# Optimization experiments

Measured on AMD Instinct MI355X. Metric: run time of the kernel, lower is better.

## Reference

```python
import jax, jax.numpy as jnp
import numpy as np

# Dims: B docs, L tokens, D hidden, H heads, NE padded entities (min_height),
# M mentions per entity, P entity pairs per doc, BLK bilinear block, NL labels.
B, L, D, H, NE, M, P = 4, 1024, 768, 12, 42, 4, 512
BLK, NL = 64, 97
OFFSET = 1  # self.offset = 1 (CLS token shift)


def setup_inputs() -> dict:
    key = jax.random.key(0)
    ks = jax.random.split(key, 10)
    sequence_output = jax.random.normal(ks[0], (B, L, D), jnp.float32)
    att = jax.random.uniform(ks[1], (B, H, L, L), jnp.float32)
    attention = att / att.sum(-1, keepdims=True)  # row-stochastic like softmax attn
    mention_pos = jax.random.randint(ks[2], (B, NE, M), 0, 1000, dtype=jnp.int32)
    hts = jax.random.randint(ks[3], (B, P, 2), 0, NE, dtype=jnp.int32)
    W_head = jax.random.normal(ks[4], (2 * D, D), jnp.float32) * 0.02
    b_head = jnp.zeros((D,), jnp.float32)
    W_tail = jax.random.normal(ks[5], (2 * D, D), jnp.float32) * 0.02
    b_tail = jnp.zeros((D,), jnp.float32)
    W_bi = jax.random.normal(ks[6], (D * BLK, NL), jnp.float32) * 0.02
    b_bi = jnp.zeros((NL,), jnp.float32)
    return dict(sequence_output=sequence_output, attention=attention,
                mention_pos=mention_pos, hts=hts,
                W_head=W_head, b_head=b_head, W_tail=W_tail, b_tail=b_tail,
                W_bi=W_bi, b_bi=b_bi)


def reference(sequence_output, attention, mention_pos, hts,
              W_head, b_head, W_tail, b_tail, W_bi, b_bi):
    pos = mention_pos + OFFSET                               # [B,NE,M]
    # --- get_hrt: entity embeds = logsumexp over mention start tokens ---
    e_emb = jax.vmap(lambda s, p: s[p])(sequence_output, pos)    # [B,NE,M,D]
    entity_embs = jax.nn.logsumexp(e_emb, axis=2)                # [B,NE,D]
    # entity attention = mean over mentions of attn rows           [B,NE,H,L]
    e_att = jax.vmap(lambda a, p: a[:, p])(attention, pos)       # [B,H,NE,M,L]
    entity_atts = e_att.mean(3).transpose(0, 2, 1, 3)            # [B,NE,H,L]
    # --- get_channel_map: ht_att = (h_att * t_att).mean(heads), normalized ---
    ht_att = jnp.einsum('bihl,bjhl->bijl', entity_atts, entity_atts) / H  # [B,NE,NE,L]
    ht_att = ht_att / (ht_att.sum(-1, keepdims=True) + 1e-5)
    rs_map = jnp.einsum('bijl,bld->bijd', ht_att, sequence_output)        # [B,NE,NE,D]
    # --- gather head/tail entity embeds and pooled context per pair ---
    h_idx, t_idx = hts[..., 0], hts[..., 1]                      # [B,P]
    hs = jnp.take_along_axis(entity_embs, h_idx[..., None], axis=1)  # [B,P,D]
    ts = jnp.take_along_axis(entity_embs, t_idx[..., None], axis=1)  # [B,P,D]
    rs = jax.vmap(lambda m, h, t: m[h, t])(rs_map, h_idx, t_idx)     # [B,P,D]
    # --- extractors + grouped bilinear classifier ---
    zs = jnp.tanh(jnp.concatenate([hs, rs], -1) @ W_head + b_head)   # [B,P,D]
    zo = jnp.tanh(jnp.concatenate([ts, rs], -1) @ W_tail + b_tail)   # [B,P,D]
    b1 = zs.reshape(B, P, D // BLK, BLK)
    b2 = zo.reshape(B, P, D // BLK, BLK)
    bl = (b1[..., :, None] * b2[..., None, :]).reshape(B, P, D * BLK)
    logits = bl @ W_bi + b_bi                                        # [B,P,NL]
    return logits
```

## Files before the change

kernel.cpp:

```cpp
#include <hip/hip_runtime.h>

constexpr int Bc = 4, Lc = 1024, Dc = 768, Hc = 12, NEc = 42, Mc = 4, Pc = 512, NLc = 97;
constexpr int BE   = Bc * NEc;
constexpr int BEp  = 176;
constexpr int ROWS = Bc * Pc;
constexpr int N2   = 2 * Dc;

typedef __attribute__((ext_vector_type(8))) short short8;
typedef _Float16 half8 __attribute__((ext_vector_type(8)));
typedef __attribute__((ext_vector_type(4))) float f32x4;

__device__ __forceinline__ f32x4 mfma_bf(short8 a, short8 b, f32x4 c) {
    return __builtin_amdgcn_mfma_f32_16x16x32_bf16(a, b, c, 0, 0, 0);
}
__device__ __forceinline__ f32x4 mfma_h(half8 a, half8 b, f32x4 c) {
    return __builtin_amdgcn_mfma_f32_16x16x32_f16(a, b, c, 0, 0, 0);
}
__device__ __forceinline__ unsigned short f2bf(float x) {
    unsigned int u = __float_as_uint(x);
    return (unsigned short)((u + 0x7fffu + ((u >> 16) & 1u)) >> 16);
}
__device__ __forceinline__ float bf2f(unsigned short h) {
    return __uint_as_float(((unsigned int)h) << 16);
}
__device__ __forceinline__ short8 ld8(const unsigned short* p) {
    return *(const short8*)(const void*)p;
}
__device__ __forceinline__ half8 ldh8(const _Float16* p) {
    return *(const half8*)(const void*)p;
}
__device__ __forceinline__ float fast_tanh(float x) {
    float cx = fminf(fmaxf(x, -9.f), 9.f);
    float u = __expf(2.f * cx);
    return 1.f - 2.f / (u + 1.f);
}


constexpr int PB_EMBS  = 0;
constexpr int PB_EATT  = PB_EMBS + BEp;
constexpr int PB_TRSEQ = PB_EATT + BE * Hc;
constexpr int PB_TRW   = PB_TRSEQ + 768;
constexpr int PB_TRWBI = PB_TRW + 576;
constexpr int PB_ZERO  = PB_TRWBI + 768;
constexpr int PB_TOTAL = PB_ZERO + 97;

__global__ __launch_bounds__(256) void k_prep(const float* __restrict__ seq,
                                              const float* __restrict__ att,
                                              const int* __restrict__ mpos,
                                              const float* __restrict__ Wh,
                                              const float* __restrict__ Wt,
                                              const float* __restrict__ wbi,
                                              unsigned short* __restrict__ ep,
                                              unsigned short* __restrict__ eatt,
                                              unsigned short* __restrict__ sp,
                                              unsigned short* __restrict__ wp1,
                                              unsigned short* __restrict__ wp2,
                                              _Float16* __restrict__ wbp,
                                              float* __restrict__ out_zero) {
    __shared__ float smem[64 * 97];
    int blk = blockIdx.x;
    int t = threadIdx.x;

    if (blk < PB_EATT) {
        int be = blk - PB_EMBS, mt = be >> 4, lm = be & 15;
        float vals[3] = {0.f, 0.f, 0.f};
        if (be < BE) {
            int b = be / NEc;
            const int* pp = mpos + be * Mc;
            int p0 = pp[0] + 1, p1 = pp[1] + 1, p2 = pp[2] + 1, p3 = pp[3] + 1;
            const float* s = seq + (size_t)b * Lc * Dc;
            #pragma unroll
            for (int i = 0; i < 3; ++i) {
                int d = t + i * 256;
                float x0 = s[(size_t)p0 * Dc + d], x1 = s[(size_t)p1 * Dc + d];
                float x2 = s[(size_t)p2 * Dc + d], x3 = s[(size_t)p3 * Dc + d];
                float mx = fmaxf(fmaxf(x0, x1), fmaxf(x2, x3));
                vals[i] = mx + logf(expf(x0 - mx) + expf(x1 - mx) + expf(x2 - mx) + expf(x3 - mx));
            }
        }
        #pragma unroll
        for (int i = 0; i < 3; ++i) {
            int d = t + i * 256;
            int idx = ((mt * 24 + (d >> 5)) << 9) + (((d >> 3) & 3) << 7) + (lm << 3) + (d & 7);
            ep[idx] = f2bf(vals[i]);
        }
    } else if (blk < PB_TRSEQ) {
        int idx = blk - PB_EATT;
        int be = idx / Hc, h = idx - be * Hc, b = be / NEc;
        const int* pp = mpos + be * Mc;
        const float* a = att + ((size_t)(b * Hc + h)) * Lc * Lc;
        const float4* r0 = (const float4*)(a + (size_t)(pp[0] + 1) * Lc);
        const float4* r1 = (const float4*)(a + (size_t)(pp[1] + 1) * Lc);
        const float4* r2 = (const float4*)(a + (size_t)(pp[2] + 1) * Lc);
        const float4* r3 = (const float4*)(a + (size_t)(pp[3] + 1) * Lc);
        unsigned short* o = eatt + ((size_t)be * Hc + h) * Lc;
        float4 v0 = r0[t], v1 = r1[t], v2 = r2[t], v3 = r3[t];
        o[t * 4 + 0] = f2bf(0.25f * (v0.x + v1.x + v2.x + v3.x));
        o[t * 4 + 1] = f2bf(0.25f * (v0.y + v1.y + v2.y + v3.y));
        o[t * 4 + 2] = f2bf(0.25f * (v0.z + v1.z + v2.z + v3.z));
        o[t * 4 + 3] = f2bf(0.25f * (v0.w + v1.w + v2.w + v3.w));
    } else if (blk < PB_TRW) {
        int idx = blk - PB_TRSEQ;
        int xb = idx & 15, yb = (idx >> 4) % 12, b = idx / 192;
        int l0 = xb * 64, d0 = yb * 64;
        const float* s = seq + (size_t)b * Lc * Dc;
        #pragma unroll
        for (int i = 0; i < 16; ++i) {
            int ii = t + i * 256, r = ii >> 6, c = ii & 63;
            smem[r * 65 + c] = s[(size_t)(l0 + r) * Dc + d0 + c];
        }
        __syncthreads();
        unsigned short* outb = sp + (size_t)b * 48 * 32 * 512;
        int flat = t * 2, lane = flat >> 3, j = flat & 7;
        #pragma unroll
        for (int nt_i = 0; nt_i < 4; ++nt_i)
            #pragma unroll
            for (int kb_i = 0; kb_i < 2; ++kb_i) {
                int kl = kb_i * 32 + (lane >> 4) * 8 + j;
                int c  = nt_i * 16 + (lane & 15);
                unsigned int v = (unsigned)f2bf(smem[kl * 65 + c]) |
                                 ((unsigned)f2bf(smem[(kl + 1) * 65 + c]) << 16);
                *(unsigned int*)&outb[(((d0 / 16 + nt_i) * 32 + (l0 / 32 + kb_i)) << 9) + flat] = v;
            }
    } else if (blk < PB_TRWBI) {
        int idx = blk - PB_TRW;
        int xb = idx % 24, yb = (idx / 24) % 12, which = idx / 288;
        int k0 = xb * 64, n0 = yb * 64;
        const float* W = which ? Wt : Wh;
        #pragma unroll
        for (int i = 0; i < 16; ++i) {
            int ii = t + i * 256, r = ii >> 6, c = ii & 63;
            smem[r * 65 + c] = W[(size_t)(k0 + r) * Dc + n0 + c];
        }
        __syncthreads();
        unsigned short* dst = (k0 < Dc) ? wp1 : wp2;
        int kb0 = ((k0 < Dc) ? k0 : (k0 - Dc)) / 32;
        int nt0 = which * 48 + n0 / 16;
        int flat = t * 2, lane = flat >> 3, j = flat & 7;
        #pragma unroll
        for (int nt_i = 0; nt_i < 4; ++nt_i)
            #pragma unroll
            for (int kb_i = 0; kb_i < 2; ++kb_i) {
                int kl = kb_i * 32 + (lane >> 4) * 8 + j;
                int c  = nt_i * 16 + (lane & 15);
                unsigned int v = (unsigned)f2bf(smem[kl * 65 + c]) |
                                 ((unsigned)f2bf(smem[(kl + 1) * 65 + c]) << 16);
                *(unsigned int*)&dst[(((nt0 + nt_i) * 24 + kb0 + kb_i) << 9) + flat] = v;
            }
    } else if (blk < PB_ZERO) {
        int idx = blk - PB_TRWBI;
        int x = idx & 63, g = idx >> 6;
        const float* src = wbi + (size_t)(g * 4096 + x * 64) * NLc;
        for (int i = t; i < 64 * NLc; i += 256) smem[i] = src[i];
        __syncthreads();
        int flat = t * 2, lane = flat >> 3, j = flat & 7;
        int lm = lane & 15, qj = (lane >> 4) * 8 + j;
        #pragma unroll
        for (int nt = 0; nt < 7; ++nt)
            #pragma unroll
            for (int half = 0; half < 2; ++half) {
                int y = half * 32 + qj;
                int n = nt * 16 + lm;
                _Float16 v0 = (n < NLc) ? (_Float16)smem[y * NLc + n] : (_Float16)0.f;
                _Float16 v1 = (n < NLc) ? (_Float16)smem[(y + 1) * NLc + n] : (_Float16)0.f;
                size_t base = ((((size_t)(nt * 12 + g) * 64 + x) * 2 + half) << 9);
                _Float16* d = wbp + base + flat;
                d[0] = v0; d[1] = v1;
            }
    } else {
        int idx = blk - PB_ZERO;
        float4* o = (float4*)(out_zero + (size_t)idx * 2048);
        float4 z = {0.f, 0.f, 0.f, 0.f};
        o[t] = z;
        o[t + 256] = z;
    }
}

__global__ __launch_bounds__(256) void k_pairw(const unsigned short* __restrict__ eatt,
                                               const int* __restrict__ hts,
                                               unsigned short* __restrict__ pwp) {
    int bp = blockIdx.x, b = bp / Pc;
    int hi = hts[bp * 2], ti = hts[bp * 2 + 1];
    const unsigned short* ai = eatt + ((size_t)(b * NEc + hi)) * Hc * Lc;
    const unsigned short* aj = eatt + ((size_t)(b * NEc + ti)) * Hc * Lc;
    int l0 = threadIdx.x * 4;
    float acc[4] = {0.f, 0.f, 0.f, 0.f};
    #pragma unroll
    for (int h = 0; h < Hc; ++h) {
        uint2 ua = *(const uint2*)(ai + h * Lc + l0);
        uint2 ub = *(const uint2*)(aj + h * Lc + l0);
        acc[0] += bf2f(ua.x & 0xffff) * bf2f(ub.x & 0xffff);
        acc[1] += bf2f(ua.x >> 16)    * bf2f(ub.x >> 16);
        acc[2] += bf2f(ua.y & 0xffff) * bf2f(ub.y & 0xffff);
        acc[3] += bf2f(ua.y >> 16)    * bf2f(ub.y >> 16);
    }
    float lsum = acc[0] + acc[1] + acc[2] + acc[3];
    #pragma unroll
    for (int off = 32; off > 0; off >>= 1) lsum += __shfl_down(lsum, off, 64);
    __shared__ float red[4];
    __shared__ float sinv;
    int lane = threadIdx.x & 63, wv = threadIdx.x >> 6;
    if (lane == 0) red[wv] = lsum;
    __syncthreads();
    if (threadIdx.x == 0) sinv = 1.f / (red[0] + red[1] + red[2] + red[3] + 1.2e-4f);
    __syncthreads();
    float s = sinv;
    unsigned short w0 = f2bf(acc[0] * s), w1 = f2bf(acc[1] * s);
    unsigned short w2 = f2bf(acc[2] * s), w3 = f2bf(acc[3] * s);
    int mt = bp >> 4, lm = bp & 15, kb = l0 >> 5, quad = (l0 >> 3) & 3, j0 = l0 & 7;
    unsigned short* dst = pwp + ((mt * 32 + kb) << 9) + (quad << 7) + (lm << 3) + j0;
    *(uint2*)dst = make_uint2((unsigned)w0 | ((unsigned)w1 << 16),
                              (unsigned)w2 | ((unsigned)w3 << 16));
}

__global__ __launch_bounds__(256) void k_rsE(const unsigned short* __restrict__ pwp,
                                             const unsigned short* __restrict__ sp,
                                             const unsigned short* __restrict__ ep,
                                             const unsigned short* __restrict__ wp1,
                                             unsigned short* __restrict__ rsp,
                                             unsigned short* __restrict__ E) {
    int tid = threadIdx.x, wave = tid >> 6, lane = tid & 63;
    int quad = lane >> 4, lm = lane & 15;
    int blk = blockIdx.x;
    if (blk < 384) {
        int mb = blk & 7, ntq = (blk >> 3) % 12, b = blk / 96;
        int nt = ntq * 4 + wave;
        int mt0 = b * 32 + mb * 4;
        const unsigned short* bbase = sp + (((size_t)b * 48 + nt) * 32 << 9) + lane * 8;
        const unsigned short* abase = pwp + ((size_t)mt0 * 32 << 9) + lane * 8;
        f32x4 acc[4] = {};
        for (int kb = 0; kb < 32; ++kb) {
            short8 bf = ld8(bbase + kb * 512);
            #pragma unroll
            for (int mf = 0; mf < 4; ++mf)
                acc[mf] = mfma_bf(ld8(abase + (mf * 32 + kb) * 512), bf, acc[mf]);
        }
        int n = nt * 16 + lm, kbo = n >> 5, lq = ((n >> 3) & 3) << 4, jo = n & 7;
        #pragma unroll
        for (int mf = 0; mf < 4; ++mf) {
            unsigned short* db = rsp + (((mt0 + mf) * 24 + kbo) << 9) + jo;
            #pragma unroll
            for (int r = 0; r < 4; ++r)
                db[(lq + quad * 4 + r) << 3] = f2bf(acc[mf][r]);
        }
    } else {
        int idx = blk - 384;
        int mt = idx % 11, ntq = idx / 11;
        int nt = ntq * 4 + wave;
        const unsigned short* ab = ep + (mt * 24 << 9) + lane * 8;
        const unsigned short* bb = wp1 + (nt * 24 << 9) + lane * 8;
        f32x4 acc = {};
        for (int kb = 0; kb < 24; ++kb)
            acc = mfma_bf(ld8(ab + kb * 512), ld8(bb + kb * 512), acc);
        #pragma unroll
        for (int r = 0; r < 4; ++r)
            E[(size_t)(mt * 16 + quad * 4 + r) * N2 + nt * 16 + lm] = f2bf(acc[r]);
    }
}

__global__ __launch_bounds__(256) void k_Rz(const unsigned short* __restrict__ rsp,
                                            const unsigned short* __restrict__ wp2,
                                            const unsigned short* __restrict__ E,
                                            const int* __restrict__ hts,
                                            const float* __restrict__ bh,
                                            const float* __restrict__ bt,
                                            _Float16* __restrict__ zs,
                                            _Float16* __restrict__ zop) {
    int tid = threadIdx.x, wave = tid >> 6, lane = tid & 63;
    int quad = lane >> 4, lm = lane & 15;
    int mt0 = blockIdx.x * 4, nt = blockIdx.y * 4 + wave;
    const unsigned short* bb = wp2 + (nt * 24 << 9) + lane * 8;
    const unsigned short* ab = rsp + ((size_t)mt0 * 24 << 9) + lane * 8;
    f32x4 acc[4] = {};
    for (int kb = 0; kb < 24; ++kb) {
        short8 bf = ld8(bb + kb * 512);
        #pragma unroll
        for (int mf = 0; mf < 4; ++mf)
            acc[mf] = mfma_bf(ld8(ab + (mf * 24 + kb) * 512), bf, acc[mf]);
    }
    int np = nt * 16 + lm;
    bool is_zs = (np < Dc);
    int n = is_zs ? np : np - Dc;
    float bias = is_zs ? bh[n] : bt[n];
    #pragma unroll
    for (int mf = 0; mf < 4; ++mf) {
        int rowbase = (mt0 + mf) * 16 + quad * 4;
        #pragma unroll
        for (int r = 0; r < 4; ++r) {
            int row = rowbase + r;
            int b = row >> 9;
            int hh = hts[row * 2], tt = hts[row * 2 + 1];
            int ent = is_zs ? hh : tt;
            float ev = bf2f(E[(size_t)(b * NEc + ent) * N2 + np]);
            float v = fast_tanh(ev + acc[mf][r] + bias);
            if (is_zs) {
                zs[(size_t)row * Dc + n] = (_Float16)v;
            } else {
                int idx = (((row >> 4) * 24 + (n >> 5)) << 9) +
                          (((((n >> 3) & 3) << 4) + (row & 15)) << 3) + (n & 7);
                zop[idx] = (_Float16)v;
            }
        }
    }
}

__global__ __launch_bounds__(256) void k_bilin(const _Float16* __restrict__ zs,
                                               const _Float16* __restrict__ zop,
                                               const _Float16* __restrict__ wbp,
                                               const float* __restrict__ bbi,
                                               float* __restrict__ out) {
    __shared__ _Float16 zlds[256 * 72];
    int tid = threadIdx.x, wave = tid >> 6, lane = tid & 63;
    int quad = lane >> 4, lm = lane & 15;
    int pb = blockIdx.x, nt = blockIdx.y, g = blockIdx.z;
    {
        const half8* src = (const half8*)(zs + ((size_t)(pb * 256 + tid)) * Dc + g * 64);
        half8* dst = (half8*)&zlds[tid * 72];
        #pragma unroll
        for (int c = 0; c < 8; ++c) dst[c] = src[c];
    }
    __syncthreads();
    int mt0 = pb * 16 + wave * 4;
    half8 zofr[4][2];
    #pragma unroll
    for (int mf = 0; mf < 4; ++mf)
        #pragma unroll
        for (int hf = 0; hf < 2; ++hf)
            zofr[mf][hf] = ldh8(zop + (((mt0 + mf) * 24 + g * 2 + hf) << 9) + lane * 8);
    const _Float16* wbase = wbp + ((size_t)(nt * 12 + g) << 16) + lane * 8;
    const _Float16* zrow = &zlds[(wave * 64 + lm) * 72];
    f32x4 acc[4] = {};
    for (int x = 0; x < 64; ++x) {
        half8 b0 = ldh8(wbase + x * 1024);
        half8 b1 = ldh8(wbase + x * 1024 + 512);
        #pragma unroll
        for (int mf = 0; mf < 4; ++mf) {
            _Float16 s = zrow[mf * 16 * 72 + x];
            half8 bc = {s, s, s, s, s, s, s, s};
            acc[mf] = mfma_h(bc * zofr[mf][0], b0, acc[mf]);
            acc[mf] = mfma_h(bc * zofr[mf][1], b1, acc[mf]);
        }
    }
    int n = nt * 16 + lm;
    if (n < NLc) {
        #pragma unroll
        for (int mf = 0; mf < 4; ++mf)
            #pragma unroll
            for (int r = 0; r < 4; ++r) {
                int row = (mt0 + mf) * 16 + quad * 4 + r;
                float v = acc[mf][r];
                if (g == 0) v += bbi[n];
                atomicAdd(out + (size_t)row * NLc + n, v);
            }
    }
}

extern "C" void kernel_launch(void* const* d_in, const int* in_sizes, int n_in,
                              void* d_out, int out_size, void* d_ws, size_t ws_size,
                              hipStream_t stream) {
    const float* seq  = (const float*)d_in[0];
    const float* att  = (const float*)d_in[1];
    const int*   mpos = (const int*)d_in[2];
    const int*   hts  = (const int*)d_in[3];
    const float* Wh   = (const float*)d_in[4];
    const float* bh   = (const float*)d_in[5];
    const float* Wt   = (const float*)d_in[6];
    const float* bt   = (const float*)d_in[7];
    const float* Wbi  = (const float*)d_in[8];
    const float* bbi  = (const float*)d_in[9];
    float* out = (float*)d_out;

    char* w = (char*)d_ws;
    unsigned short* embs_p = (unsigned short*)(w);
    unsigned short* eatt_b = (unsigned short*)(w + 270336);
    unsigned short* pw_p   = (unsigned short*)(w + 4399104);
    unsigned short* seq_p  = (unsigned short*)(w + 8593408);
    _Float16*       wbi_p  = (_Float16*)(w + 14884864);
    unsigned short* wp1    = (unsigned short*)(w + 25894912);
    unsigned short* wp2    = (unsigned short*)(w + 28254208);
    unsigned short* E      = (unsigned short*)(w + 30613504);
    unsigned short* rs_p   = (unsigned short*)(w + 31154176);
    _Float16*       zs     = (_Float16*)(w + 34299904);
    _Float16*       zo_p   = (_Float16*)(w + 37445632);

    k_prep <<<PB_TOTAL, 256, 0, stream>>>(seq, att, mpos, Wh, Wt, Wbi,
                                          embs_p, eatt_b, seq_p, wp1, wp2, wbi_p, out);
    k_pairw<<<ROWS, 256, 0, stream>>>(eatt_b, hts, pw_p);
    k_rsE  <<<648, 256, 0, stream>>>(pw_p, seq_p, embs_p, wp1, rs_p, E);
    k_Rz   <<<dim3(32, 24), 256, 0, stream>>>(rs_p, wp2, E, hts, bh, bt, zs, zo_p);
    k_bilin<<<dim3(8, 7, 12), 256, 0, stream>>>(zs, zo_p, wbi_p, bbi, out);
}
```

Baseline: 372.2 us.

## Fuse four post-prep kernels into one cooperative persistent kernel with grid syncs

Replaces the pairwise-weight, rs/E GEMM, extractor, and bilinear kernel launches with a single cooperative kernel that loops over each stage's tasks and separates stages with grid-wide barriers. The grid size comes from an occupancy query, capped at 768 blocks, and the old four-launch path is kept as a fallback if the cooperative launch fails. This removes three kernel launch gaps and the tail drain between stages. In exchange, each stage runs with a fixed persistent grid that may be smaller than the original launch, grid.sync adds barrier cost, and the shared-memory union may lower occupancy.

New measurement: 594.3 us. +59.7%, slower.

```diff
diff --git a/kernel.cpp b/kernel.cpp
--- a/kernel.cpp
+++ b/kernel.cpp
@@ -1,4 +1,7 @@
 #include <hip/hip_runtime.h>
+#include <hip/hip_cooperative_groups.h>
+
+namespace cg = cooperative_groups;
 
 constexpr int Bc = 4, Lc = 1024, Dc = 768, Hc = 12, NEc = 42, Mc = 4, Pc = 512, NLc = 97;
 constexpr int BE   = Bc * NEc;
@@ -355,6 +358,190 @@
     }
 }
 
+__global__ __launch_bounds__(256) void k_main(
+        const unsigned short* __restrict__ eatt,
+        const int* __restrict__ hts,
+        unsigned short* __restrict__ pwp,
+        const unsigned short* __restrict__ sp,
+        const unsigned short* __restrict__ ep,
+        const unsigned short* __restrict__ wp1,
+        unsigned short* __restrict__ rsp,
+        unsigned short* __restrict__ E,
+        const unsigned short* __restrict__ wp2,
+        const float* __restrict__ bh,
+        const float* __restrict__ bt,
+        _Float16* __restrict__ zs,
+        _Float16* __restrict__ zop,
+        const _Float16* __restrict__ wbp,
+        const float* __restrict__ bbi,
+        float* __restrict__ out) {
+    cg::grid_group gridg = cg::this_grid();
+    __shared__ union alignas(16) {
+        _Float16 h16[256 * 72];
+        struct { float red[4]; float sinv; } pw;
+    } sm;
+    int tid = threadIdx.x, bid = blockIdx.x;
+    int nblk = gridDim.x;
+    int wave = tid >> 6, lane = tid & 63;
+    int quad = lane >> 4, lm = lane & 15;
+
+    for (int bp = bid; bp < ROWS; bp += nblk) {
+        __syncthreads();
+        int b = bp / Pc;
+        int hi = hts[bp * 2], ti = hts[bp * 2 + 1];
+        const unsigned short* ai = eatt + ((size_t)(b * NEc + hi)) * Hc * Lc;
+        const unsigned short* aj = eatt + ((size_t)(b * NEc + ti)) * Hc * Lc;
+        int l0 = tid * 4;
+        float acc[4] = {0.f, 0.f, 0.f, 0.f};
+        #pragma unroll
+        for (int h = 0; h < Hc; ++h) {
+            uint2 ua = *(const uint2*)(ai + h * Lc + l0);
+            uint2 ub = *(const uint2*)(aj + h * Lc + l0);
+            acc[0] += bf2f(ua.x & 0xffff) * bf2f(ub.x & 0xffff);
+            acc[1] += bf2f(ua.x >> 16)    * bf2f(ub.x >> 16);
+            acc[2] += bf2f(ua.y & 0xffff) * bf2f(ub.y & 0xffff);
+            acc[3] += bf2f(ua.y >> 16)    * bf2f(ub.y >> 16);
+        }
+        float lsum = acc[0] + acc[1] + acc[2] + acc[3];
+        #pragma unroll
+        for (int off = 32; off > 0; off >>= 1) lsum += __shfl_down(lsum, off, 64);
+        if (lane == 0) sm.pw.red[wave] = lsum;
+        __syncthreads();
+        if (tid == 0)
+            sm.pw.sinv = 1.f / (sm.pw.red[0] + sm.pw.red[1] + sm.pw.red[2] + sm.pw.red[3] + 1.2e-4f);
+        __syncthreads();
+        float s = sm.pw.sinv;
+        unsigned short w0 = f2bf(acc[0] * s), w1 = f2bf(acc[1] * s);
+        unsigned short w2 = f2bf(acc[2] * s), w3 = f2bf(acc[3] * s);
+        int mt = bp >> 4, plm = bp & 15, kb = l0 >> 5, pq = (l0 >> 3) & 3, j0 = l0 & 7;
+        unsigned short* dst = pwp + ((mt * 32 + kb) << 9) + (pq << 7) + (plm << 3) + j0;
+        *(uint2*)dst = make_uint2((unsigned)w0 | ((unsigned)w1 << 16),
+                                  (unsigned)w2 | ((unsigned)w3 << 16));
+    }
+    gridg.sync();
+
+    for (int blk = bid; blk < 648; blk += nblk) {
+        if (blk < 384) {
+            int mb = blk & 7, ntq = (blk >> 3) % 12, b = blk / 96;
+            int nt = ntq * 4 + wave;
+            int mt0 = b * 32 + mb * 4;
+            const unsigned short* bbase = sp + (((size_t)b * 48 + nt) * 32 << 9) + lane * 8;
+            const unsigned short* abase = pwp + ((size_t)mt0 * 32 << 9) + lane * 8;
+            f32x4 acc[4] = {};
+            for (int kb = 0; kb < 32; ++kb) {
+                short8 bf = ld8(bbase + kb * 512);
+                #pragma unroll
+                for (int mf = 0; mf < 4; ++mf)
+                    acc[mf] = mfma_bf(ld8(abase + (mf * 32 + kb) * 512), bf, acc[mf]);
+            }
+            int n = nt * 16 + lm, kbo = n >> 5, lq = ((n >> 3) & 3) << 4, jo = n & 7;
+            #pragma unroll
+            for (int mf = 0; mf < 4; ++mf) {
+                unsigned short* db = rsp + (((mt0 + mf) * 24 + kbo) << 9) + jo;
+                #pragma unroll
+                for (int r = 0; r < 4; ++r)
+                    db[(lq + quad * 4 + r) << 3] = f2bf(acc[mf][r]);
+            }
+        } else {
+            int idx = blk - 384;
+            int mt = idx % 11, ntq = idx / 11;
+            int nt = ntq * 4 + wave;
+            const unsigned short* ab = ep + (mt * 24 << 9) + lane * 8;
+            const unsigned short* bb = wp1 + (nt * 24 << 9) + lane * 8;
+            f32x4 acc = {};
+            for (int kb = 0; kb < 24; ++kb)
+                acc = mfma_bf(ld8(ab + kb * 512), ld8(bb + kb * 512), acc);
+            #pragma unroll
+            for (int r = 0; r < 4; ++r)
+                E[(size_t)(mt * 16 + quad * 4 + r) * N2 + nt * 16 + lm] = f2bf(acc[r]);
+        }
+    }
+    gridg.sync();
+
+    for (int task = bid; task < 768; task += nblk) {
+        int mt0 = (task & 31) * 4, nt = (task >> 5) * 4 + wave;
+        const unsigned short* bb = wp2 + (nt * 24 << 9) + lane * 8;
+        const unsigned short* ab = rsp + ((size_t)mt0 * 24 << 9) + lane * 8;
+        f32x4 acc[4] = {};
+        for (int kb = 0; kb < 24; ++kb) {
+            short8 bf = ld8(bb + kb * 512);
+            #pragma unroll
+            for (int mf = 0; mf < 4; ++mf)
+                acc[mf] = mfma_bf(ld8(ab + (mf * 24 + kb) * 512), bf, acc[mf]);
+        }
+        int np = nt * 16 + lm;
+        bool is_zs = (np < Dc);
+        int n = is_zs ? np : np - Dc;
+        float bias = is_zs ? bh[n] : bt[n];
+        #pragma unroll
+        for (int mf = 0; mf < 4; ++mf) {
+            int rowbase = (mt0 + mf) * 16 + quad * 4;
+            #pragma unroll
+            for (int r = 0; r < 4; ++r) {
+                int row = rowbase + r;
+                int b = row >> 9;
+                int hh = hts[row * 2], tt = hts[row * 2 + 1];
+                int ent = is_zs ? hh : tt;
+                float ev = bf2f(E[(size_t)(b * NEc + ent) * N2 + np]);
+                float v = fast_tanh(ev + acc[mf][r] + bias);
+                if (is_zs) {
+                    zs[(size_t)row * Dc + n] = (_Float16)v;
+                } else {
+                    int idx = (((row >> 4) * 24 + (n >> 5)) << 9) +
+                              (((((n >> 3) & 3) << 4) + (row & 15)) << 3) + (n & 7);
+                    zop[idx] = (_Float16)v;
+                }
+            }
+        }
+    }
+    gridg.sync();
+
+    for (int task = bid; task < 672; task += nblk) {
+        int pb = task & 7, nt = (task >> 3) % 7, g = task / 56;
+        __syncthreads();
+        {
+            const half8* src = (const half8*)(zs + ((size_t)(pb * 256 + tid)) * Dc + g * 64);
+            half8* dst = (half8*)&sm.h16[tid * 72];
+            #pragma unroll
+            for (int c = 0; c < 8; ++c) dst[c] = src[c];
+        }
+        __syncthreads();
+        int mt0 = pb * 16 + wave * 4;
+        half8 zofr[4][2];
+        #pragma unroll
+        for (int mf = 0; mf < 4; ++mf)
+            #pragma unroll
+            for (int hf = 0; hf < 2; ++hf)
+                zofr[mf][hf] = ldh8(zop + (((mt0 + mf) * 24 + g * 2 + hf) << 9) + lane * 8);
+        const _Float16* wbase = wbp + ((size_t)(nt * 12 + g) << 16) + lane * 8;
+        const _Float16* zrow = &sm.h16[(wave * 64 + lm) * 72];
+        f32x4 acc[4] = {};
+        for (int x = 0; x < 64; ++x) {
+            half8 b0 = ldh8(wbase + x * 1024);
+            half8 b1 = ldh8(wbase + x * 1024 + 512);
+            #pragma unroll
+            for (int mf = 0; mf < 4; ++mf) {
+                _Float16 s = zrow[mf * 16 * 72 + x];
+                half8 bc = {s, s, s, s, s, s, s, s};
+                acc[mf] = mfma_h(bc * zofr[mf][0], b0, acc[mf]);
+                acc[mf] = mfma_h(bc * zofr[mf][1], b1, acc[mf]);
+            }
+        }
+        int n = nt * 16 + lm;
+        if (n < NLc) {
+            #pragma unroll
+            for (int mf = 0; mf < 4; ++mf)
+                #pragma unroll
+                for (int r = 0; r < 4; ++r) {
+                    int row = (mt0 + mf) * 16 + quad * 4 + r;
+                    float v = acc[mf][r];
+                    if (g == 0) v += bbi[n];
+                    atomicAdd(out + (size_t)row * NLc + n, v);
+                }
+        }
+    }
+}
+
 extern "C" void kernel_launch(void* const* d_in, const int* in_sizes, int n_in,
                               void* d_out, int out_size, void* d_ws, size_t ws_size,
                               hipStream_t stream) {
@@ -383,10 +570,28 @@
     _Float16*       zs     = (_Float16*)(w + 34299904);
     _Float16*       zo_p   = (_Float16*)(w + 37445632);
 
-    k_prep <<<PB_TOTAL, 256, 0, stream>>>(seq, att, mpos, Wh, Wt, Wbi,
-                                          embs_p, eatt_b, seq_p, wp1, wp2, wbi_p, out);
-    k_pairw<<<ROWS, 256, 0, stream>>>(eatt_b, hts, pw_p);
-    k_rsE  <<<648, 256, 0, stream>>>(pw_p, seq_p, embs_p, wp1, rs_p, E);
-    k_Rz   <<<dim3(32, 24), 256, 0, stream>>>(rs_p, wp2, E, hts, bh, bt, zs, zo_p);
-    k_bilin<<<dim3(8, 7, 12), 256, 0, stream>>>(zs, zo_p, wbi_p, bbi, out);
-}
+    k_prep<<<PB_TOTAL, 256, 0, stream>>>(seq, att, mpos, Wh, Wt, Wbi,
+                                         embs_p, eatt_b, seq_p, wp1, wp2, wbi_p, out);
+
+    int perCU = 0;
+    hipError_t qe = hipOccupancyMaxActiveBlocksPerMultiprocessor(&perCU, k_main, 256, 0);
+    int cgb = (qe == hipSuccess && perCU > 0) ? perCU * 256 : 512;
+    if (cgb > 768) cgb = 768;
+
+    void* kargs[] = {
+        (void*)&eatt_b, (void*)&hts, (void*)&pw_p,
+        (void*)&seq_p, (void*)&embs_p, (void*)&wp1,
+        (void*)&rs_p, (void*)&E,
+        (void*)&wp2, (void*)&bh, (void*)&bt,
+        (void*)&zs, (void*)&zo_p,
+        (void*)&wbi_p, (void*)&bbi, (void*)&out
+    };
+    hipError_t le = hipLaunchCooperativeKernel((void*)k_main, dim3(cgb), dim3(256),
+                                               kargs, 0, stream);
+    if (le != hipSuccess) {
+        k_pairw<<<ROWS, 256, 0, stream>>>(eatt_b, hts, pw_p);
+        k_rsE  <<<648, 256, 0, stream>>>(pw_p, seq_p, embs_p, wp1, rs_p, E);
+        k_Rz   <<<dim3(32, 24), 256, 0, stream>>>(rs_p, wp2, E, hts, bh, bt, zs, zo_p);
+        k_bilin<<<dim3(8, 7, 12), 256, 0, stream>>>(zs, zo_p, wbi_p, bbi, out);
+    }
+}
```
